# Kernel optimization log

Hardware: AMD Instinct MI355X
Metric: run time of the kernel (lower is better)

The kernel has to match this reference:

```python
import jax, jax.numpy as jnp
import numpy as np

B, T, D, H = 32, 512, 512, 512
P_IN, P_HID = 0.2, 0.2  # input_dropout, hidden_dropout


def _dropout_mask(key, shape, p):
    # inverted dropout mask, as torch F.dropout applied to a ones tensor
    keep = jax.random.bernoulli(key, 1.0 - p, shape)
    return keep.astype(jnp.float32) / (1.0 - p)


def setup_inputs() -> dict:
    key = jax.random.key(0)
    ks = jax.random.split(key, 12)
    k = 1.0 / np.sqrt(H)
    u = lambda kk, shp: jax.random.uniform(kk, shp, jnp.float32, -k, k)
    inp = {
        "x": jax.random.normal(ks[0], (B, T, D), jnp.float32),
        # variational dropout masks (sampled once, reused every timestep)
        "mask_x": _dropout_mask(ks[1], (B, D), P_IN),
        "mask_out": _dropout_mask(ks[2], (B, 2 * H), P_HID),
        "mask_h": jnp.stack([_dropout_mask(ks[3], (B, H), P_HID),
                             _dropout_mask(ks[4], (B, H), P_HID)]),  # [n_layers,B,H]
        # layer 0 (input D), 2 directions stacked; LSTM gate order i,f,g,o
        "w_ih_l0": u(ks[5], (2, 4 * H, D)),
        "w_hh_l0": u(ks[6], (2, 4 * H, H)),
        "b_l0": u(ks[7], (2, 4 * H)),
        # layer 1 (input 2H)
        "w_ih_l1": u(ks[8], (2, 4 * H, 2 * H)),
        "w_hh_l1": u(ks[9], (2, 4 * H, H)),
        "b_l1": u(ks[10], (2, 4 * H)),
    }
    return inp


def _lstm_scan(x_seq, w_ih, w_hh, b, mask_h, reverse):
    # x_seq: [T,B,in]; variational dropout mask_h applied to h each step
    b_, h_ = x_seq.shape[1], w_hh.shape[1]
    h0 = jnp.zeros((b_, h_), x_seq.dtype)

    def step(carry, x_t):
        h, c = carry
        gates = x_t @ w_ih.T + (h * mask_h) @ w_hh.T + b
        i, f, g, o = jnp.split(gates, 4, axis=-1)
        c = jax.nn.sigmoid(f) * c + jax.nn.sigmoid(i) * jnp.tanh(g)
        h = jax.nn.sigmoid(o) * jnp.tanh(c)
        return (h, c), h

    (hT, cT), ys = jax.lax.scan(step, (h0, h0), x_seq, reverse=reverse)
    return ys, hT, cT  # ys in original time order even when reverse


def reference(x, mask_x, mask_out, mask_h, w_ih_l0, w_hh_l0, b_l0,
              w_ih_l1, w_hh_l1, b_l1):
    xt = jnp.swapaxes(x, 0, 1)  # [T,B,D] (batch_first transpose)
    layers = [(w_ih_l0, w_hh_l0, b_l0), (w_ih_l1, w_hh_l1, b_l1)]
    hs, cs = [], []
    inp = xt * mask_x[None]  # layer-0 input mask
    for li, (wi, wh, bb) in enumerate(layers):
        outs = []
        for d in range(2):  # forward / backward direction
            ys, hT, cT = _lstm_scan(inp, wi[d], wh[d], bb[d], mask_h[li],
                                    reverse=(d == 1))
            outs.append(ys)
            hs.append(hT)
            cs.append(cT)
        inp = jnp.concatenate(outs, axis=-1)  # [T,B,2H]
        if li + 1 < len(layers):
            inp = inp * mask_out[None]  # mask applied as next layer's input mask
    output = jnp.swapaxes(inp, 0, 1)  # [B,T,2H]
    hn = jnp.stack(hs)  # [num_layers*2, B, H]
    cn = jnp.stack(cs)
    return output, hn, cn
```

## Files before the change

### kernel.cpp

```cpp
#include <hip/hip_runtime.h>
#include <math.h>

typedef unsigned short ushort_t;
typedef short short8 __attribute__((ext_vector_type(8)));
typedef float floatx4 __attribute__((ext_vector_type(4)));
typedef float float4v __attribute__((ext_vector_type(4)));
typedef unsigned int uint4v __attribute__((ext_vector_type(4)));

__device__ __forceinline__ float b2f(ushort_t u) {
    union { unsigned int i; float f; } v; v.i = ((unsigned int)u) << 16; return v.f;
}
__device__ __forceinline__ ushort_t f2b(float f) {
    union { float f; unsigned int i; } v; v.f = f;
    unsigned int x = v.i;
    return (ushort_t)((x + 0x7fffu + ((x >> 16) & 1u)) >> 16);
}
__device__ __forceinline__ void split8(const float* v, short8& hi, short8& lo) {
#pragma unroll
    for (int e = 0; e < 8; ++e) {
        ushort_t h = f2b(v[e]);
        hi[e] = (short)h;
        lo[e] = (short)f2b(v[e] - b2f(h));
    }
}
__device__ __forceinline__ void load8f(const float* p, float* v) {
    *(float4v*)(v)     = *(const float4v*)(p);
    *(float4v*)(v + 4) = *(const float4v*)(p + 4);
}
__device__ __forceinline__ floatx4 mfma16(short8 a, short8 b, floatx4 c) {
    return __builtin_amdgcn_mfma_f32_16x16x32_bf16(a, b, c, 0, 0, 0);
}
__device__ __forceinline__ void store2_cc(void* p, ushort_t v) {
    asm volatile("global_store_short %0, %1, off sc0 sc1"
                 :: "v"(p), "v"((unsigned int)v) : "memory");
}

__global__ void detect_dtype(const unsigned int* __restrict__ x, int* __restrict__ flag) {
    __shared__ int cnt;
    if (threadIdx.x == 0) cnt = 0;
    __syncthreads();
    int c = 0;
#pragma unroll
    for (int i = 0; i < 8; ++i) {
        unsigned int w = x[threadIdx.x * 8 + i];
        unsigned int e = (w >> 7) & 0xFFu;
        if (e >= 100u && e <= 140u) ++c;
    }
    atomicAdd(&cnt, c);
    __syncthreads();
    if (threadIdx.x == 0) *flag = (cnt > 1024) ? 1 : 0;
}

__global__ __launch_bounds__(256) void prep(
    const int* __restrict__ flag,
    const void* __restrict__ x, const void* __restrict__ mask_x,
    char* __restrict__ xs)
{
    const bool isbf = (*flag != 0);
    const int i = blockIdx.x * 256 + threadIdx.x;
    const int b = i >> 15;
    const int rem = i & 32767;
    const int t = rem >> 6;
    const int c = rem & 63;
    const size_t xoff = ((size_t)(b * 512 + t)) * 512 + c * 8;
    if (isbf) {
        const ushort_t* X = (const ushort_t*)x;
        const ushort_t* M = (const ushort_t*)mask_x + b * 512 + c * 8;
        short8 o;
#pragma unroll
        for (int e = 0; e < 8; ++e) o[e] = (short)f2b(b2f(X[xoff + e]) * b2f(M[e]));
        *(short8*)(xs + ((size_t)t * 32 + b) * 1024 + c * 16) = o;
    } else {
        float v[8], m[8];
        load8f((const float*)x + xoff, v);
        load8f((const float*)mask_x + b * 512 + c * 8, m);
#pragma unroll
        for (int e = 0; e < 8; ++e) v[e] *= m[e];
        short8 hi, lo; split8(v, hi, lo);
        char* p = xs + ((size_t)t * 32 + b) * 2048 + c * 32;
        *(short8*)p = hi; *(short8*)(p + 16) = lo;
    }
}

__device__ __forceinline__ int lds_swz(int row, int o) {
    return o ^ ((row & 7) << 4) ^ (((o >> 6) & 7) << 4);
}

template <int LAYER>
__global__ __launch_bounds__(512, 2) void lstm_phase(
    const int* __restrict__ flag,
    const char* __restrict__ xs,
    char* __restrict__ os,
    char* __restrict__ hs,
    unsigned int* cnt,
    const void* __restrict__ w_ih, const void* __restrict__ w_hh,
    const void* __restrict__ bias, const void* __restrict__ mask_h,
    const void* __restrict__ mask_out, void* __restrict__ dout,
    int os4_host, int write_hn)
{
    __shared__ __align__(16) char smem[40960];
    float* gb = (float*)(smem + 32768);
    const int dir  = blockIdx.x >> 6;
    const int b6   = blockIdx.x & 63;
    const int jt   = b6 & 31;
    const int m    = b6 >> 5;
    const int j0   = jt << 4;
    const int tid  = threadIdx.x;
    const int w    = tid >> 6;
    const int q    = w & 3;
    const int kh   = w >> 2;
    const int lane = tid & 63;
    const int n16  = lane & 15;
    const int quad = lane >> 4;
    const bool isbf = (*flag != 0);
    const bool os4  = (!isbf) && (os4_host != 0);
    unsigned int* mycnt = cnt + dir * 16;
    constexpr int KI = (LAYER == 0) ? 512 : 1024;
    constexpr int NI = KI / 64;
    constexpr int NH = 8;
    const int gq = q * 512 + j0 + n16;

    short8 wih_h[NI], wih_l[NI], whh_h[NH], whh_l[NH];
    if (isbf) {
        const ushort_t* WI = (const ushort_t*)w_ih + ((size_t)(dir * 2048 + gq)) * KI + kh * (KI / 2) + quad * 8;
        const ushort_t* WH = (const ushort_t*)w_hh + ((size_t)(dir * 2048 + gq)) * 512 + kh * 256 + quad * 8;
#pragma unroll
        for (int ki = 0; ki < NI; ++ki) { wih_h[ki] = *(const short8*)(WI + ki * 32); wih_l[ki] = short8{0,0,0,0,0,0,0,0}; }
#pragma unroll
        for (int ki = 0; ki < NH; ++ki) { whh_h[ki] = *(const short8*)(WH + ki * 32); whh_l[ki] = short8{0,0,0,0,0,0,0,0}; }
    } else {
        const float* WI = (const float*)w_ih + ((size_t)(dir * 2048 + gq)) * KI + kh * (KI / 2) + quad * 8;
        const float* WH = (const float*)w_hh + ((size_t)(dir * 2048 + gq)) * 512 + kh * 256 + quad * 8;
#pragma unroll
        for (int ki = 0; ki < NI; ++ki) { float w8[8]; load8f(WI + ki * 32, w8); split8(w8, wih_h[ki], wih_l[ki]); }
#pragma unroll
        for (int ki = 0; ki < NH; ++ki) { float w8[8]; load8f(WH + ki * 32, w8); split8(w8, whh_h[ki], whh_l[ki]); }
    }

    float pbi = 0.f, pbf = 0.f, pbg = 0.f, pbo = 0.f, pmh = 0.f, pmo = 0.f;
    int eb = 0, en = 0, ej = 0, erow = 0;
    if (tid < 256) {
        eb = tid >> 4; en = tid & 15; ej = j0 + en; erow = m * 16 + eb;
        if (isbf) {
            const ushort_t* BI = (const ushort_t*)bias;
            const ushort_t* MH = (const ushort_t*)mask_h + LAYER * 16384;
            pbi = b2f(BI[dir * 2048 + ej]);        pbf = b2f(BI[dir * 2048 + 512 + ej]);
            pbg = b2f(BI[dir * 2048 + 1024 + ej]); pbo = b2f(BI[dir * 2048 + 1536 + ej]);
            pmh = b2f(MH[erow * 512 + ej]);
            if (LAYER == 0) pmo = b2f(((const ushort_t*)mask_out)[erow * 1024 + dir * 512 + ej]);
        } else {
            const float* BI = (const float*)bias;
            const float* MH = (const float*)mask_h + LAYER * 16384;
            pbi = BI[dir * 2048 + ej];        pbf = BI[dir * 2048 + 512 + ej];
            pbg = BI[dir * 2048 + 1024 + ej]; pbo = BI[dir * 2048 + 1536 + ej];
            pmh = MH[erow * 512 + ej];
            if (LAYER == 0) pmo = ((const float*)mask_out)[erow * 1024 + dir * 512 + ej];
        }
    }
    float creg = 0.f;

    for (int s = 0; s < 512; ++s) {
        const int t = dir ? (511 - s) : s;
        floatx4 acc = {0.f, 0.f, 0.f, 0.f};

        if (isbf) {
            const int stride = (LAYER == 0) ? 1024 : 2048;
            const char* xb = xs + ((size_t)t * 32 + m * 16 + n16) * stride + (kh * NI * 4 + quad) * 16;
#pragma unroll
            for (int ki = 0; ki < NI; ++ki) {
                short8 a = *(const short8*)(xb + ki * 64);
                acc = mfma16(a, wih_h[ki], acc);
            }
        } else if (LAYER == 1 && !os4) {
            const char* xb = xs + ((size_t)t * 32 + m * 16 + n16) * 2048 + (kh * 64 + quad) * 16;
#pragma unroll
            for (int ki = 0; ki < NI; ++ki) {
                short8 a = *(const short8*)(xb + ki * 64);
                acc = mfma16(a, wih_h[ki], acc);
                acc = mfma16(a, wih_l[ki], acc);
            }
        } else {
            const int stride = (LAYER == 0) ? 2048 : 4096;
            const char* xb = xs + ((size_t)t * 32 + m * 16 + n16) * stride + (kh * NI * 4 + quad) * 32;
#pragma unroll
            for (int ki = 0; ki < NI; ++ki) {
                short8 ah = *(const short8*)(xb + ki * 128);
                short8 al = *(const short8*)(xb + ki * 128 + 16);
                acc = mfma16(ah, wih_h[ki], acc);
                acc = mfma16(al, wih_h[ki], acc);
                acc = mfma16(ah, wih_l[ki], acc);
            }
        }

        if (tid == 0) {
            const unsigned int target = 64u * (unsigned int)s;
            while (__hip_atomic_load(mycnt, __ATOMIC_RELAXED, __HIP_MEMORY_SCOPE_AGENT) < target) { }
        }
        __syncthreads();
        __builtin_amdgcn_sched_barrier(0);

        {
            const char* hr = hs + (size_t)((s & 1) * 2 + dir) * 65536;
            const int planes = isbf ? 1 : 2;
            if (tid < planes * 256) {
                const int p = tid >> 8, v = tid & 255;
                const int row = v >> 4, seg = v & 15;
                const char* gsrc = hr + p * 32768 + (size_t)(m * 16 + row) * 1024 + seg * 64;
                uint4v t0, t1, t2, t3;
                asm volatile("global_load_dwordx4 %0, %1, off sc0 sc1" : "=v"(t0) : "v"(gsrc));
                asm volatile("global_load_dwordx4 %0, %1, off sc0 sc1" : "=v"(t1) : "v"(gsrc + 16));
                asm volatile("global_load_dwordx4 %0, %1, off sc0 sc1" : "=v"(t2) : "v"(gsrc + 32));
                asm volatile("global_load_dwordx4 %0, %1, off sc0 sc1" : "=v"(t3) : "v"(gsrc + 48));
                asm volatile("s_waitcnt vmcnt(0)" ::: "memory");
                __builtin_amdgcn_sched_barrier(0);
                char* lbase = smem + p * 16384 + row * 1024;
                *(uint4v*)(lbase + lds_swz(row, seg * 64))      = t0;
                *(uint4v*)(lbase + lds_swz(row, seg * 64 + 16)) = t1;
                *(uint4v*)(lbase + lds_swz(row, seg * 64 + 32)) = t2;
                *(uint4v*)(lbase + lds_swz(row, seg * 64 + 48)) = t3;
            }
        }
        __syncthreads();

        {
            const char* hrow = smem + n16 * 1024;
            if (isbf) {
#pragma unroll
                for (int ki = 0; ki < NH; ++ki) {
                    const int o = kh * 512 + ki * 64 + quad * 16;
                    short8 ah = *(const short8*)(hrow + lds_swz(n16, o));
                    acc = mfma16(ah, whh_h[ki], acc);
                }
            } else {
#pragma unroll
                for (int ki = 0; ki < NH; ++ki) {
                    const int o = kh * 512 + ki * 64 + quad * 16;
                    const int so = lds_swz(n16, o);
                    short8 ah = *(const short8*)(hrow + so);
                    short8 al = *(const short8*)(hrow + 16384 + so);
                    acc = mfma16(ah, whh_h[ki], acc);
                    acc = mfma16(al, whh_h[ki], acc);
                    acc = mfma16(ah, whh_l[ki], acc);
                }
            }
        }

#pragma unroll
        for (int r = 0; r < 4; ++r)
            gb[((q * 2 + kh) * 16 + quad * 4 + r) * 16 + n16] = acc[r];
        __syncthreads();

        if (tid < 256) {
            const int cidx = eb * 16 + en;
            float ig = gb[0 * 256 + cidx] + gb[1 * 256 + cidx] + pbi;
            float fg = gb[2 * 256 + cidx] + gb[3 * 256 + cidx] + pbf;
            float gg = gb[4 * 256 + cidx] + gb[5 * 256 + cidx] + pbg;
            float og = gb[6 * 256 + cidx] + gb[7 * 256 + cidx] + pbo;
            float si = 1.f / (1.f + expf(-ig));
            float sf = 1.f / (1.f + expf(-fg));
            float so = 1.f / (1.f + expf(-og));
            float cn = sf * creg + si * tanhf(gg);
            float h  = so * tanhf(cn);
            creg = cn;

            const int jg = dir * 512 + ej;
            float hm = h * pmh;
            char* hw = hs + (size_t)(((s + 1) & 1) * 2 + dir) * 65536 + (size_t)erow * 1024 + ej * 2;
            ushort_t hhi = f2b(hm);
            store2_cc(hw, hhi);
            if (!isbf) store2_cc(hw + 32768, f2b(hm - b2f(hhi)));

            if constexpr (LAYER == 0) {
                float ho = h * pmo;
                if (os4) {
                    char* op = os + ((size_t)t * 32 + erow) * 4096 + (jg >> 3) * 32 + (jg & 7) * 2;
                    ushort_t ohi = f2b(ho);
                    *(ushort_t*)op        = ohi;
                    *(ushort_t*)(op + 16) = f2b(ho - b2f(ohi));
                } else {
                    *(ushort_t*)(os + ((size_t)t * 32 + erow) * 2048 + (size_t)jg * 2) = f2b(ho);
                }
            } else {
                size_t o1 = ((size_t)erow * 512 + t) * 1024 + jg;
                if (isbf) ((ushort_t*)dout)[o1] = f2b(h);
                else      ((float*)dout)[o1]    = h;
            }
            if (s == 511 && write_hn) {
                size_t hnidx = 16777216u + (size_t)((LAYER * 2 + dir) * 32 + erow) * 512 + ej;
                if (isbf) { ((ushort_t*)dout)[hnidx] = f2b(h); ((ushort_t*)dout)[hnidx + 65536] = f2b(cn); }
                else      { ((float*)dout)[hnidx]    = h;      ((float*)dout)[hnidx + 65536]    = cn; }
            }
        }
        asm volatile("s_waitcnt vmcnt(0)" ::: "memory");
        __syncthreads();
        if (tid == 0)
            __hip_atomic_fetch_add(mycnt, 1u, __ATOMIC_RELAXED, __HIP_MEMORY_SCOPE_AGENT);
    }
}

extern "C" void kernel_launch(void* const* d_in, const int* in_sizes, int n_in,
                              void* d_out, int out_size, void* d_ws, size_t ws_size,
                              hipStream_t stream) {
    char* ws = (char*)d_ws;
    const size_t HSB = 262144;
    int os4 = (ws_size >= 67108864ull + HSB + 512) ? 1 : 0;
    size_t osb = os4 ? 67108864ull : 33554432ull;
    char* hs = ws + osb;
    unsigned int* cnt = (unsigned int*)(hs + HSB);
    int* flag = (int*)(hs + HSB + 256);
    int write_hn = (out_size >= 16908288) ? 1 : 0;

    int hb = -1;
    if (in_sizes && n_in > 0) {
        if (in_sizes[0] == 33554432) hb = 0;
        else if (in_sizes[0] == 16777216) hb = 1;
    }

    hipMemsetAsync(hs, 0, HSB + 512, stream);
    if (hb == 1)       hipMemsetAsync(flag, 1, 4, stream);
    else if (hb == -1) detect_dtype<<<1, 256, 0, stream>>>((const unsigned int*)d_in[0], flag);

    prep<<<4096, 256, 0, stream>>>(flag, d_in[0], d_in[1], (char*)d_out);

    lstm_phase<0><<<128, 512, 0, stream>>>(flag, (const char*)d_out, ws,
        hs, cnt, d_in[4], d_in[5], d_in[6], d_in[3], d_in[2], d_out,
        os4, write_hn);

    hipMemsetAsync(hs, 0, HSB + 256, stream);

    lstm_phase<1><<<128, 512, 0, stream>>>(flag, (const char*)ws, ws,
        hs, cnt, d_in[7], d_in[8], d_in[9], d_in[3], nullptr, d_out,
        os4, write_hn);
}
```

Measured before the change: 8.607 ms.

## Replace atomic counter barrier with per-block flags, prefetch input projection, vectorize epilogue

Swaps the shared atomic-counter grid barrier for per-block step flags. Each block publishes its step with one store, and a whole wavefront polls all 32 peer flags in parallel, which removes atomic contention and the single-thread spin plus block barrier. The input-projection MFMAs for the next timestep now run after the current step's epilogue, taking them off the critical path between barriers. The gate epilogue moves to a single wave that handles 4 columns per lane with packed 8-byte stores. This cuts store count but serializes the elementwise work onto 64 lanes.

```diff
diff --git a/kernel.cpp b/kernel.cpp
--- a/kernel.cpp
+++ b/kernel.cpp
@@ -30,9 +30,13 @@
 __device__ __forceinline__ floatx4 mfma16(short8 a, short8 b, floatx4 c) {
     return __builtin_amdgcn_mfma_f32_16x16x32_bf16(a, b, c, 0, 0, 0);
 }
-__device__ __forceinline__ void store2_cc(void* p, ushort_t v) {
-    asm volatile("global_store_short %0, %1, off sc0 sc1"
-                 :: "v"(p), "v"((unsigned int)v) : "memory");
+__device__ __forceinline__ void store8_cc(void* p, unsigned long long v) {
+    asm volatile("global_store_dwordx2 %0, %1, off sc0 sc1"
+                 :: "v"(p), "v"(v) : "memory");
+}
+__device__ __forceinline__ void store4_cc(void* p, unsigned int v) {
+    asm volatile("global_store_dword %0, %1, off sc0 sc1"
+                 :: "v"(p), "v"(v) : "memory");
 }
 
 __global__ void detect_dtype(const unsigned int* __restrict__ x, int* __restrict__ flag) {
@@ -92,7 +96,7 @@
     const char* __restrict__ xs,
     char* __restrict__ os,
     char* __restrict__ hs,
-    unsigned int* cnt,
+    char* __restrict__ flags,
     const void* __restrict__ w_ih, const void* __restrict__ w_hh,
     const void* __restrict__ bias, const void* __restrict__ mask_h,
     const void* __restrict__ mask_out, void* __restrict__ dout,
@@ -114,89 +118,81 @@
     const int quad = lane >> 4;
     const bool isbf = (*flag != 0);
     const bool os4  = (!isbf) && (os4_host != 0);
-    unsigned int* mycnt = cnt + dir * 16;
     constexpr int KI = (LAYER == 0) ? 512 : 1024;
-    constexpr int NI = KI / 64;
+    constexpr int NI = KI / 128;
+    constexpr int NIT = (KI / 2) / 32;
     constexpr int NH = 8;
     const int gq = q * 512 + j0 + n16;
-
-    short8 wih_h[NI], wih_l[NI], whh_h[NH], whh_l[NH];
+    (void)NI;
+
+    short8 wih_h[NIT], wih_l[NIT], whh_h[NH], whh_l[NH];
     if (isbf) {
         const ushort_t* WI = (const ushort_t*)w_ih + ((size_t)(dir * 2048 + gq)) * KI + kh * (KI / 2) + quad * 8;
         const ushort_t* WH = (const ushort_t*)w_hh + ((size_t)(dir * 2048 + gq)) * 512 + kh * 256 + quad * 8;
 #pragma unroll
-        for (int ki = 0; ki < NI; ++ki) { wih_h[ki] = *(const short8*)(WI + ki * 32); wih_l[ki] = short8{0,0,0,0,0,0,0,0}; }
+        for (int ki = 0; ki < NIT; ++ki) { wih_h[ki] = *(const short8*)(WI + ki * 32); wih_l[ki] = short8{0,0,0,0,0,0,0,0}; }
 #pragma unroll
         for (int ki = 0; ki < NH; ++ki) { whh_h[ki] = *(const short8*)(WH + ki * 32); whh_l[ki] = short8{0,0,0,0,0,0,0,0}; }
     } else {
         const float* WI = (const float*)w_ih + ((size_t)(dir * 2048 + gq)) * KI + kh * (KI / 2) + quad * 8;
         const float* WH = (const float*)w_hh + ((size_t)(dir * 2048 + gq)) * 512 + kh * 256 + quad * 8;
 #pragma unroll
-        for (int ki = 0; ki < NI; ++ki) { float w8[8]; load8f(WI + ki * 32, w8); split8(w8, wih_h[ki], wih_l[ki]); }
+        for (int ki = 0; ki < NIT; ++ki) { float w8[8]; load8f(WI + ki * 32, w8); split8(w8, wih_h[ki], wih_l[ki]); }
 #pragma unroll
         for (int ki = 0; ki < NH; ++ki) { float w8[8]; load8f(WH + ki * 32, w8); split8(w8, whh_h[ki], whh_l[ki]); }
     }
 
-    float pbi = 0.f, pbf = 0.f, pbg = 0.f, pbo = 0.f, pmh = 0.f, pmo = 0.f;
-    int eb = 0, en = 0, ej = 0, erow = 0;
-    if (tid < 256) {
-        eb = tid >> 4; en = tid & 15; ej = j0 + en; erow = m * 16 + eb;
+    auto xpart = [&](int ts) -> floatx4 {
+        floatx4 a = {0.f, 0.f, 0.f, 0.f};
         if (isbf) {
-            const ushort_t* BI = (const ushort_t*)bias;
-            const ushort_t* MH = (const ushort_t*)mask_h + LAYER * 16384;
-            pbi = b2f(BI[dir * 2048 + ej]);        pbf = b2f(BI[dir * 2048 + 512 + ej]);
-            pbg = b2f(BI[dir * 2048 + 1024 + ej]); pbo = b2f(BI[dir * 2048 + 1536 + ej]);
-            pmh = b2f(MH[erow * 512 + ej]);
-            if (LAYER == 0) pmo = b2f(((const ushort_t*)mask_out)[erow * 1024 + dir * 512 + ej]);
+            const int stride = (LAYER == 0) ? 1024 : 2048;
+            const char* xb = xs + ((size_t)ts * 32 + m * 16 + n16) * stride + (kh * NIT * 4 + quad) * 16;
+#pragma unroll
+            for (int ki = 0; ki < NIT; ++ki)
+                a = mfma16(*(const short8*)(xb + ki * 64), wih_h[ki], a);
+        } else if (LAYER == 1 && !os4) {
+            const char* xb = xs + ((size_t)ts * 32 + m * 16 + n16) * 2048 + (kh * 64 + quad) * 16;
+#pragma unroll
+            for (int ki = 0; ki < NIT; ++ki) {
+                short8 av = *(const short8*)(xb + ki * 64);
+                a = mfma16(av, wih_h[ki], a);
+                a = mfma16(av, wih_l[ki], a);
+            }
         } else {
-            const float* BI = (const float*)bias;
-            const float* MH = (const float*)mask_h + LAYER * 16384;
-            pbi = BI[dir * 2048 + ej];        pbf = BI[dir * 2048 + 512 + ej];
-            pbg = BI[dir * 2048 + 1024 + ej]; pbo = BI[dir * 2048 + 1536 + ej];
-            pmh = MH[erow * 512 + ej];
-            if (LAYER == 0) pmo = ((const float*)mask_out)[erow * 1024 + dir * 512 + ej];
-        }
-    }
-    float creg = 0.f;
+            const int stride = (LAYER == 0) ? 2048 : 4096;
+            const char* xb = xs + ((size_t)ts * 32 + m * 16 + n16) * stride + (kh * NIT * 4 + quad) * 32;
+#pragma unroll
+            for (int ki = 0; ki < NIT; ++ki) {
+                short8 ah = *(const short8*)(xb + ki * 128);
+                short8 al = *(const short8*)(xb + ki * 128 + 16);
+                a = mfma16(ah, wih_h[ki], a);
+                a = mfma16(al, wih_h[ki], a);
+                a = mfma16(ah, wih_l[ki], a);
+            }
+        }
+        return a;
+    };
+
+    const int el4 = (lane & 3) * 4;
+    const int erow = m * 16 + (lane >> 2);
+    const int ej0 = j0 + el4;
+    float creg[4] = {0.f, 0.f, 0.f, 0.f};
+
+    const char* myflags = flags + (size_t)((dir * 2 + m) * 32) * 64;
+    floatx4 acc = xpart(dir ? 511 : 0);
 
     for (int s = 0; s < 512; ++s) {
         const int t = dir ? (511 - s) : s;
-        floatx4 acc = {0.f, 0.f, 0.f, 0.f};
-
-        if (isbf) {
-            const int stride = (LAYER == 0) ? 1024 : 2048;
-            const char* xb = xs + ((size_t)t * 32 + m * 16 + n16) * stride + (kh * NI * 4 + quad) * 16;
-#pragma unroll
-            for (int ki = 0; ki < NI; ++ki) {
-                short8 a = *(const short8*)(xb + ki * 64);
-                acc = mfma16(a, wih_h[ki], acc);
-            }
-        } else if (LAYER == 1 && !os4) {
-            const char* xb = xs + ((size_t)t * 32 + m * 16 + n16) * 2048 + (kh * 64 + quad) * 16;
-#pragma unroll
-            for (int ki = 0; ki < NI; ++ki) {
-                short8 a = *(const short8*)(xb + ki * 64);
-                acc = mfma16(a, wih_h[ki], acc);
-                acc = mfma16(a, wih_l[ki], acc);
-            }
-        } else {
-            const int stride = (LAYER == 0) ? 2048 : 4096;
-            const char* xb = xs + ((size_t)t * 32 + m * 16 + n16) * stride + (kh * NI * 4 + quad) * 32;
-#pragma unroll
-            for (int ki = 0; ki < NI; ++ki) {
-                short8 ah = *(const short8*)(xb + ki * 128);
-                short8 al = *(const short8*)(xb + ki * 128 + 16);
-                acc = mfma16(ah, wih_h[ki], acc);
-                acc = mfma16(al, wih_h[ki], acc);
-                acc = mfma16(ah, wih_l[ki], acc);
-            }
-        }
-
-        if (tid == 0) {
-            const unsigned int target = 64u * (unsigned int)s;
-            while (__hip_atomic_load(mycnt, __ATOMIC_RELAXED, __HIP_MEMORY_SCOPE_AGENT) < target) { }
-        }
-        __syncthreads();
+
+        {
+            const char* fb = myflags + (size_t)(lane & 31) * 64;
+            int fv;
+            for (;;) {
+                asm volatile("global_load_dword %0, %1, off sc0 sc1\n\ts_waitcnt vmcnt(0)"
+                             : "=v"(fv) : "v"(fb) : "memory");
+                if (__all(fv >= s)) break;
+            }
+        }
         __builtin_amdgcn_sched_barrier(0);
 
         {
@@ -228,8 +224,7 @@
 #pragma unroll
                 for (int ki = 0; ki < NH; ++ki) {
                     const int o = kh * 512 + ki * 64 + quad * 16;
-                    short8 ah = *(const short8*)(hrow + lds_swz(n16, o));
-                    acc = mfma16(ah, whh_h[ki], acc);
+                    acc = mfma16(*(const short8*)(hrow + lds_swz(n16, o)), whh_h[ki], acc);
                 }
             } else {
 #pragma unroll
@@ -250,51 +245,108 @@
             gb[((q * 2 + kh) * 16 + quad * 4 + r) * 16 + n16] = acc[r];
         __syncthreads();
 
-        if (tid < 256) {
-            const int cidx = eb * 16 + en;
-            float ig = gb[0 * 256 + cidx] + gb[1 * 256 + cidx] + pbi;
-            float fg = gb[2 * 256 + cidx] + gb[3 * 256 + cidx] + pbf;
-            float gg = gb[4 * 256 + cidx] + gb[5 * 256 + cidx] + pbg;
-            float og = gb[6 * 256 + cidx] + gb[7 * 256 + cidx] + pbo;
-            float si = 1.f / (1.f + expf(-ig));
-            float sf = 1.f / (1.f + expf(-fg));
-            float so = 1.f / (1.f + expf(-og));
-            float cn = sf * creg + si * tanhf(gg);
-            float h  = so * tanhf(cn);
-            creg = cn;
-
-            const int jg = dir * 512 + ej;
-            float hm = h * pmh;
-            char* hw = hs + (size_t)(((s + 1) & 1) * 2 + dir) * 65536 + (size_t)erow * 1024 + ej * 2;
-            ushort_t hhi = f2b(hm);
-            store2_cc(hw, hhi);
-            if (!isbf) store2_cc(hw + 32768, f2b(hm - b2f(hhi)));
-
+        if (w == 7) {
+            float4v gA[8];
+#pragma unroll
+            for (int z = 0; z < 8; ++z)
+                gA[z] = *(const float4v*)(gb + z * 256 + lane * 4);
+
+            float bi4[4], bf4[4], bg4[4], bo4[4], mh4[4], mo4[4];
+            if (isbf) {
+                const ushort_t* BI = (const ushort_t*)bias;
+                const ushort_t* MH = (const ushort_t*)mask_h + LAYER * 16384;
+#pragma unroll
+                for (int u = 0; u < 4; ++u) {
+                    const int ej = ej0 + u;
+                    bi4[u] = b2f(BI[dir * 2048 + ej]);        bf4[u] = b2f(BI[dir * 2048 + 512 + ej]);
+                    bg4[u] = b2f(BI[dir * 2048 + 1024 + ej]); bo4[u] = b2f(BI[dir * 2048 + 1536 + ej]);
+                    mh4[u] = b2f(MH[erow * 512 + ej]);
+                    mo4[u] = (LAYER == 0) ? b2f(((const ushort_t*)mask_out)[erow * 1024 + dir * 512 + ej]) : 0.f;
+                }
+            } else {
+                const float* BI = (const float*)bias;
+                const float* MH = (const float*)mask_h + LAYER * 16384;
+                *(float4v*)bi4 = *(const float4v*)(BI + dir * 2048 + ej0);
+                *(float4v*)bf4 = *(const float4v*)(BI + dir * 2048 + 512 + ej0);
+                *(float4v*)bg4 = *(const float4v*)(BI + dir * 2048 + 1024 + ej0);
+                *(float4v*)bo4 = *(const float4v*)(BI + dir * 2048 + 1536 + ej0);
+                *(float4v*)mh4 = *(const float4v*)(MH + erow * 512 + ej0);
+                if (LAYER == 0) *(float4v*)mo4 = *(const float4v*)((const float*)mask_out + erow * 1024 + dir * 512 + ej0);
+            }
+
+            float hv4[4], cn4[4];
+            unsigned long long hiw = 0ull, low = 0ull;
+#pragma unroll
+            for (int u = 0; u < 4; ++u) {
+                float ig = gA[0][u] + gA[1][u] + bi4[u];
+                float fg = gA[2][u] + gA[3][u] + bf4[u];
+                float gg = gA[4][u] + gA[5][u] + bg4[u];
+                float og = gA[6][u] + gA[7][u] + bo4[u];
+                float si = 1.f / (1.f + expf(-ig));
+                float sf = 1.f / (1.f + expf(-fg));
+                float so = 1.f / (1.f + expf(-og));
+                float cn = sf * creg[u] + si * tanhf(gg);
+                float h  = so * tanhf(cn);
+                creg[u] = cn; hv4[u] = h; cn4[u] = cn;
+                float hm = h * mh4[u];
+                ushort_t hhi = f2b(hm);
+                hiw |= (unsigned long long)hhi << (16 * u);
+                low |= (unsigned long long)f2b(hm - b2f(hhi)) << (16 * u);
+            }
+            char* hw = hs + (size_t)(((s + 1) & 1) * 2 + dir) * 65536 + (size_t)erow * 1024 + ej0 * 2;
+            store8_cc(hw, hiw);
+            if (!isbf) store8_cc(hw + 32768, low);
+
+            const int jg0 = dir * 512 + ej0;
             if constexpr (LAYER == 0) {
-                float ho = h * pmo;
+                unsigned long long ohi = 0ull, olo = 0ull;
+#pragma unroll
+                for (int u = 0; u < 4; ++u) {
+                    float ho = hv4[u] * mo4[u];
+                    ushort_t oh = f2b(ho);
+                    ohi |= (unsigned long long)oh << (16 * u);
+                    olo |= (unsigned long long)f2b(ho - b2f(oh)) << (16 * u);
+                }
                 if (os4) {
-                    char* op = os + ((size_t)t * 32 + erow) * 4096 + (jg >> 3) * 32 + (jg & 7) * 2;
-                    ushort_t ohi = f2b(ho);
-                    *(ushort_t*)op        = ohi;
-                    *(ushort_t*)(op + 16) = f2b(ho - b2f(ohi));
+                    char* op = os + ((size_t)t * 32 + erow) * 4096 + (jg0 >> 3) * 32 + (jg0 & 7) * 2;
+                    *(unsigned long long*)op = ohi;
+                    *(unsigned long long*)(op + 16) = olo;
                 } else {
-                    *(ushort_t*)(os + ((size_t)t * 32 + erow) * 2048 + (size_t)jg * 2) = f2b(ho);
+                    *(unsigned long long*)(os + ((size_t)t * 32 + erow) * 2048 + (size_t)jg0 * 2) = ohi;
                 }
             } else {
-                size_t o1 = ((size_t)erow * 512 + t) * 1024 + jg;
-                if (isbf) ((ushort_t*)dout)[o1] = f2b(h);
-                else      ((float*)dout)[o1]    = h;
+                size_t o1 = ((size_t)erow * 512 + t) * 1024 + jg0;
+                if (isbf) {
+                    unsigned long long ow = 0ull;
+#pragma unroll
+                    for (int u = 0; u < 4; ++u) ow |= (unsigned long long)f2b(hv4[u]) << (16 * u);
+                    *(unsigned long long*)((ushort_t*)dout + o1) = ow;
+                } else {
+                    *(float4v*)((float*)dout + o1) = float4v{hv4[0], hv4[1], hv4[2], hv4[3]};
+                }
             }
             if (s == 511 && write_hn) {
-                size_t hnidx = 16777216u + (size_t)((LAYER * 2 + dir) * 32 + erow) * 512 + ej;
-                if (isbf) { ((ushort_t*)dout)[hnidx] = f2b(h); ((ushort_t*)dout)[hnidx + 65536] = f2b(cn); }
-                else      { ((float*)dout)[hnidx]    = h;      ((float*)dout)[hnidx + 65536]    = cn; }
-            }
-        }
-        asm volatile("s_waitcnt vmcnt(0)" ::: "memory");
-        __syncthreads();
-        if (tid == 0)
-            __hip_atomic_fetch_add(mycnt, 1u, __ATOMIC_RELAXED, __HIP_MEMORY_SCOPE_AGENT);
+                size_t hnidx = 16777216u + (size_t)((LAYER * 2 + dir) * 32 + erow) * 512 + ej0;
+                if (isbf) {
+                    unsigned long long hw_ = 0ull, cw_ = 0ull;
+#pragma unroll
+                    for (int u = 0; u < 4; ++u) {
+                        hw_ |= (unsigned long long)f2b(hv4[u]) << (16 * u);
+                        cw_ |= (unsigned long long)f2b(cn4[u]) << (16 * u);
+                    }
+                    *(unsigned long long*)((ushort_t*)dout + hnidx) = hw_;
+                    *(unsigned long long*)((ushort_t*)dout + hnidx + 65536) = cw_;
+                } else {
+                    *(float4v*)((float*)dout + hnidx) = float4v{hv4[0], hv4[1], hv4[2], hv4[3]};
+                    *(float4v*)((float*)dout + hnidx + 65536) = float4v{cn4[0], cn4[1], cn4[2], cn4[3]};
+                }
+            }
+            asm volatile("s_waitcnt vmcnt(0)" ::: "memory");
+            if (lane == 0)
+                store4_cc((void*)(myflags + (size_t)jt * 64), (unsigned int)(s + 1));
+        }
+
+        if (s != 511) acc = xpart(dir ? (510 - s) : (s + 1));
     }
 }
 
@@ -303,11 +355,12 @@
                               hipStream_t stream) {
     char* ws = (char*)d_ws;
     const size_t HSB = 262144;
-    int os4 = (ws_size >= 67108864ull + HSB + 512) ? 1 : 0;
+    const size_t FLB = 8192;
+    int os4 = (ws_size >= 67108864ull + HSB + FLB + 64) ? 1 : 0;
     size_t osb = os4 ? 67108864ull : 33554432ull;
     char* hs = ws + osb;
-    unsigned int* cnt = (unsigned int*)(hs + HSB);
-    int* flag = (int*)(hs + HSB + 256);
+    char* flags = hs + HSB;
+    int* flag = (int*)(flags + FLB);
     int write_hn = (out_size >= 16908288) ? 1 : 0;
 
     int hb = -1;
@@ -316,19 +369,19 @@
         else if (in_sizes[0] == 16777216) hb = 1;
     }
 
-    hipMemsetAsync(hs, 0, HSB + 512, stream);
+    hipMemsetAsync(hs, 0, HSB + FLB + 64, stream);
     if (hb == 1)       hipMemsetAsync(flag, 1, 4, stream);
     else if (hb == -1) detect_dtype<<<1, 256, 0, stream>>>((const unsigned int*)d_in[0], flag);
 
     prep<<<4096, 256, 0, stream>>>(flag, d_in[0], d_in[1], (char*)d_out);
 
     lstm_phase<0><<<128, 512, 0, stream>>>(flag, (const char*)d_out, ws,
-        hs, cnt, d_in[4], d_in[5], d_in[6], d_in[3], d_in[2], d_out,
+        hs, flags, d_in[4], d_in[5], d_in[6], d_in[3], d_in[2], d_out,
         os4, write_hn);
 
-    hipMemsetAsync(hs, 0, HSB + 256, stream);
+    hipMemsetAsync(hs, 0, HSB + FLB, stream);
 
     lstm_phase<1><<<128, 512, 0, stream>>>(flag, (const char*)ws, ws,
-        hs, cnt, d_in[7], d_in[8], d_in[9], d_in[3], nullptr, d_out,
+        hs, flags, d_in[7], d_in[8], d_in[9], d_in[3], nullptr, d_out,
         os4, write_hn);
 }
```

Measured after the change: 9.330 ms. +8.4%, slower.
